# Kernel tuning notes

Measured on AMD Instinct MI355X. Metric: run time of the kernel, lower is better.

Reference implementation:

```python
import jax, jax.numpy as jnp
import numpy as np

N_NODES = 100000
N_EDGES = 1600000
IN_FEATS = 256
OUT_FEATS = 128


def setup_inputs() -> dict:
    key = jax.random.key(0)
    k1, k2, k3, k4 = jax.random.split(key, 4)
    feat = jax.random.normal(k1, (N_NODES, IN_FEATS), dtype=jnp.float32)
    # Glorot-uniform-like weight
    limit = np.sqrt(6.0 / (IN_FEATS + OUT_FEATS)).astype(np.float32)
    weight = jax.random.uniform(k2, (IN_FEATS, OUT_FEATS), dtype=jnp.float32,
                                minval=-limit, maxval=limit)
    bias = jnp.zeros((OUT_FEATS,), dtype=jnp.float32)
    src = jax.random.randint(k3, (N_EDGES,), 0, N_NODES, dtype=jnp.int32)
    dst = jax.random.randint(k4, (N_EDGES,), 0, N_NODES, dtype=jnp.int32)
    return {"feat": feat, "weight": weight, "bias": bias, "src": src, "dst": dst}


def reference(feat, weight, bias, src, dst):
    n = feat.shape[0]
    # in-degree per node (edges point src -> dst), clipped to >= 1
    deg = jax.ops.segment_sum(jnp.ones_like(dst, dtype=feat.dtype), dst,
                              num_segments=n)
    norm = jnp.clip(deg, 1.0, None) ** -0.5          # [N]
    norm = norm[:, None]                             # [N, 1]
    h = feat * norm                                  # src-side normalization
    # in_feats > out_feats: project first, then aggregate (cheaper messages)
    h = h @ weight                                   # [N, out]
    agg = jax.ops.segment_sum(h[src], dst, num_segments=n)  # sparse sum-aggregate
    rst = agg * norm + bias                          # dst-side norm + bias
    return rst
```

## Files before the change

### kernel.cpp

```cpp
#include <hip/hip_runtime.h>

#define IN_F 256
#define OUT_F 128
#define BSH 7
#define BNODES 128
#define MAXBUCK 1024
#define BIN1A_BLOCKS 256
#define BIN1B_BLOCKS 256

typedef short bf16x8 __attribute__((ext_vector_type(8)));
typedef float f32x4 __attribute__((ext_vector_type(4)));

__device__ inline unsigned short f2bf(float x) {
    union { float f; unsigned u; } v; v.f = x;
    unsigned r = v.u + 0x7FFFu + ((v.u >> 16) & 1u);
    return (unsigned short)(r >> 16);
}
__device__ inline float bf2f(unsigned short x) {
    union { unsigned u; float f; } v; v.u = ((unsigned)x) << 16;
    return v.f;
}

__global__ __launch_bounds__(256) void prep_kernel(const float* __restrict__ W,
                                                   unsigned short* __restrict__ Wt,
                                                   const int* __restrict__ dst,
                                                   int* __restrict__ bhist,
                                                   int n_edges, int nbuck) {
    if ((int)blockIdx.x < BIN1A_BLOCKS) {
        __shared__ int hist[MAXBUCK];
        const int tid = threadIdx.x;
        const int chunk = (n_edges + BIN1A_BLOCKS - 1) / BIN1A_BLOCKS;
        const int lo = blockIdx.x * chunk;
        const int hi = min(lo + chunk, n_edges);

        for (int i = tid; i < MAXBUCK; i += 256) hist[i] = 0;
        __syncthreads();
        for (int e = lo + tid; e < hi; e += 256)
            atomicAdd(&hist[dst[e] >> BSH], 1);
        __syncthreads();
        for (int i = tid; i < nbuck; i += 256) {
            int c = hist[i];
            if (c) atomicAdd(&bhist[i], c);
        }
    } else {
        int n = blockIdx.x - BIN1A_BLOCKS;
        int k = threadIdx.x;
        Wt[n * IN_F + k] = f2bf(W[k * OUT_F + n]);
    }
}

__global__ __launch_bounds__(1024) void scanb_kernel(const int* __restrict__ bhist,
                                                     int* __restrict__ bstart,
                                                     int* __restrict__ gcur,
                                                     int* __restrict__ rstart,
                                                     int nbuck, int n_nodes) {
    __shared__ int sh[1024];
    int tid = threadIdx.x;
    int v = (tid < nbuck) ? bhist[tid] : 0;
    sh[tid] = v;
    __syncthreads();
    #pragma unroll
    for (int off = 1; off < 1024; off <<= 1) {
        int t = (tid >= off) ? sh[tid - off] : 0;
        __syncthreads();
        sh[tid] += t;
        __syncthreads();
    }
    int ex = sh[tid] - v;
    if (tid < nbuck) { bstart[tid] = ex; gcur[tid] = ex; }
    if (tid == 1023) {
        bstart[nbuck] = sh[1023];
        rstart[n_nodes] = sh[1023];
    }
}

__global__ __launch_bounds__(512) void gemm_bin_kernel(
        const float* __restrict__ feat, const unsigned short* __restrict__ Wt,
        unsigned short* __restrict__ h, int n_nodes,
        const int* __restrict__ src, const int* __restrict__ dst,
        int* __restrict__ gcur, unsigned* __restrict__ ebuf,
        int n_edges, int nbuck) {

    __shared__ __align__(16) char smem[65536];

    if ((int)blockIdx.x < BIN1B_BLOCKS) {
        int* hist  = (int*)smem;
        int* lbase = hist + MAXBUCK;
        const int tid = threadIdx.x;
        const int chunk = (n_edges + BIN1B_BLOCKS - 1) / BIN1B_BLOCKS;
        const int lo = blockIdx.x * chunk;
        const int hi = min(lo + chunk, n_edges);

        for (int i = tid; i < nbuck; i += 512) hist[i] = 0;
        __syncthreads();
        for (int e = lo + tid; e < hi; e += 512)
            atomicAdd(&hist[dst[e] >> BSH], 1);
        __syncthreads();
        for (int i = tid; i < nbuck; i += 512) {
            int c = hist[i];
            lbase[i] = (c > 0) ? atomicAdd(&gcur[i], c) : 0;
            hist[i] = 0;
        }
        __syncthreads();
        for (int e = lo + tid; e < hi; e += 512) {
            int d = dst[e];
            int bkt = d >> BSH;
            int off = atomicAdd(&hist[bkt], 1);
            ebuf[lbase[bkt] + off] = ((unsigned)src[e] << BSH) | (unsigned)(d & (BNODES - 1));
        }
    } else {
        unsigned short* Bs = (unsigned short*)smem;

        const int tid  = threadIdx.x;
        const int wave = tid >> 6;
        const int lane = tid & 63;
        const int gb   = blockIdx.x - BIN1B_BLOCKS;
        const int r0   = (gb * 8 + wave) * 16;
        const int lrow = lane & 15;
        const int g    = lane >> 4;
        const int kgrp = g * 8;

        {
            const f32x4* srcv = reinterpret_cast<const f32x4*>(Wt);
            f32x4* dstv = reinterpret_cast<f32x4*>(Bs);
            #pragma unroll
            for (int i = 0; i < 8; ++i) {
                int c   = tid + i * 512;
                int row = c >> 5;
                int col = c & 31;
                dstv[c] = srcv[row * 32 + (col ^ (row & 7))];
            }
        }

        const int row  = r0 + lrow;
        const int rowc = (row < n_nodes) ? row : (n_nodes - 1);
        const float* arow = feat + (size_t)rowc * IN_F;

        f32x4 a[16];
        #pragma unroll
        for (int k0 = 0; k0 < IN_F / 32; ++k0) {
            a[2 * k0]     = *reinterpret_cast<const f32x4*>(arow + k0 * 32 + kgrp);
            a[2 * k0 + 1] = *reinterpret_cast<const f32x4*>(arow + k0 * 32 + kgrp + 4);
        }
        asm volatile("" ::
            "v"(a[0]),  "v"(a[1]),  "v"(a[2]),  "v"(a[3]),
            "v"(a[4]),  "v"(a[5]),  "v"(a[6]),  "v"(a[7]),
            "v"(a[8]),  "v"(a[9]),  "v"(a[10]), "v"(a[11]),
            "v"(a[12]), "v"(a[13]), "v"(a[14]), "v"(a[15]));

        __syncthreads();

        f32x4 acc[8];
        #pragma unroll
        for (int n = 0; n < 8; ++n) acc[n] = (f32x4){0.f, 0.f, 0.f, 0.f};

        const bf16x8* bsv = reinterpret_cast<const bf16x8*>(Bs);

        #pragma unroll
        for (int k0 = 0; k0 < IN_F / 32; ++k0) {
            const f32x4 a0 = a[2 * k0];
            const f32x4 a1 = a[2 * k0 + 1];
            bf16x8 afr;
            afr[0] = (short)f2bf(a0[0]);
            afr[1] = (short)f2bf(a0[1]);
            afr[2] = (short)f2bf(a0[2]);
            afr[3] = (short)f2bf(a0[3]);
            afr[4] = (short)f2bf(a1[0]);
            afr[5] = (short)f2bf(a1[1]);
            afr[6] = (short)f2bf(a1[2]);
            afr[7] = (short)f2bf(a1[3]);
            #pragma unroll
            for (int n = 0; n < 8; ++n) {
                const int brow = n * 16 + lrow;
                bf16x8 bfr = bsv[brow * 32 + ((k0 * 4 + g) ^ (brow & 7))];
                acc[n] = __builtin_amdgcn_mfma_f32_16x16x32_bf16(afr, bfr, acc[n], 0, 0, 0);
            }
        }

        const int orow0 = r0 + g * 4;
        #pragma unroll
        for (int n = 0; n < 8; ++n) {
            #pragma unroll
            for (int j = 0; j < 4; ++j) {
                int orow = orow0 + j;
                if (orow < n_nodes)
                    h[(size_t)orow * OUT_F + n * 16 + lrow] = f2bf(acc[n][j]);
            }
        }
    }
}

__global__ __launch_bounds__(256) void bin2_kernel(const unsigned* __restrict__ ebuf,
                                                   const int* __restrict__ bstart,
                                                   int* __restrict__ rstart,
                                                   float* __restrict__ norm,
                                                   int* __restrict__ eidx,
                                                   int n_nodes) {
    __shared__ int lcnt[BNODES];
    __shared__ int lex[BNODES];
    const int tid = threadIdx.x;
    const int node0 = blockIdx.x << BSH;
    const int e0 = bstart[blockIdx.x];
    const int e1 = bstart[blockIdx.x + 1];

    if (tid < BNODES) lcnt[tid] = 0;
    __syncthreads();
    for (int e = e0 + tid; e < e1; e += 256)
        atomicAdd(&lcnt[ebuf[e] & (BNODES - 1)], 1);
    __syncthreads();

    int own = (tid < BNODES) ? lcnt[tid] : 0;
    if (tid < BNODES) lex[tid] = own;
    __syncthreads();
    #pragma unroll
    for (int off = 1; off < BNODES; off <<= 1) {
        int t = (tid >= off && tid < BNODES) ? lex[tid - off] : 0;
        __syncthreads();
        if (tid < BNODES) lex[tid] += t;
        __syncthreads();
    }
    if (tid < BNODES) {
        int ex = lex[tid] - own;
        lex[tid] = ex;
        int g = node0 + tid;
        if (g <= n_nodes) rstart[g] = e0 + ex;
        if (g < n_nodes) {
            float d = (float)own;
            if (d < 1.0f) d = 1.0f;
            norm[g] = 1.0f / sqrtf(d);
        }
        lcnt[tid] = 0;
    }
    __syncthreads();

    for (int e = e0 + tid; e < e1; e += 256) {
        unsigned pk = ebuf[e];
        int dl = pk & (BNODES - 1);
        int pos = atomicAdd(&lcnt[dl], 1);
        eidx[e0 + lex[dl] + pos] = (int)(pk >> BSH);
    }
}

__global__ __launch_bounds__(256) void agg_kernel(const unsigned short* __restrict__ h,
                                                  const int* __restrict__ eidx,
                                                  const int* __restrict__ rstart,
                                                  const float* __restrict__ norm,
                                                  const float* __restrict__ bias,
                                                  float* __restrict__ out,
                                                  int n_nodes) {
    const int wave = threadIdx.x >> 6;
    const int lane = threadIdx.x & 63;
    const int node = blockIdx.x * 4 + wave;
    if (node >= n_nodes) return;

    const int start = rstart[node];
    const int cnt   = rstart[node + 1] - start;

    float a0 = 0.f, a1 = 0.f;
    for (int base = 0; base < cnt; base += 64) {
        const int rem = min(64, cnt - base);
        int   ev = (lane < rem) ? eidx[start + base + lane] : 0;
        float nv = (lane < rem) ? norm[ev] : 0.f;

        int j = 0;
        for (; j + 8 <= rem; j += 8) {
            unsigned v[8];
            float    nn[8];
            #pragma unroll
            for (int q = 0; q < 8; ++q) {
                int s = __shfl(ev, j + q);
                nn[q] = __shfl(nv, j + q);
                v[q]  = *reinterpret_cast<const unsigned*>(h + (size_t)s * OUT_F + lane * 2);
            }
            #pragma unroll
            for (int q = 0; q < 8; ++q) {
                a0 += bf2f((unsigned short)(v[q] & 0xffffu)) * nn[q];
                a1 += bf2f((unsigned short)(v[q] >> 16))     * nn[q];
            }
        }
        for (; j < rem; ++j) {
            int   s  = __shfl(ev, j);
            float nm = __shfl(nv, j);
            unsigned v = *reinterpret_cast<const unsigned*>(h + (size_t)s * OUT_F + lane * 2);
            a0 += bf2f((unsigned short)(v & 0xffffu)) * nm;
            a1 += bf2f((unsigned short)(v >> 16))     * nm;
        }
    }

    const float nd = norm[node];
    float2 r;
    r.x = a0 * nd + bias[lane * 2];
    r.y = a1 * nd + bias[lane * 2 + 1];
    *reinterpret_cast<float2*>(out + (size_t)node * OUT_F + lane * 2) = r;
}

extern "C" void kernel_launch(void* const* d_in, const int* in_sizes, int n_in,
                              void* d_out, int out_size, void* d_ws, size_t ws_size,
                              hipStream_t stream) {
    const float* feat   = (const float*)d_in[0];
    const float* weight = (const float*)d_in[1];
    const float* bias   = (const float*)d_in[2];
    const int*   src    = (const int*)d_in[3];
    const int*   dst    = (const int*)d_in[4];
    float* out = (float*)d_out;

    const int n_nodes = in_sizes[0] / IN_F;
    const int n_edges = in_sizes[3];
    const int nbuck   = (n_nodes + BNODES - 1) >> BSH;
    const int gemm_blocks = (n_nodes + 127) / 128;

    char* ws = (char*)d_ws;
    size_t off = 0;
    auto alloc = [&](size_t bytes) {
        char* p = ws + off;
        off += (bytes + 15) & ~(size_t)15;
        return p;
    };
    unsigned short* h  = (unsigned short*)alloc((size_t)n_nodes * OUT_F * 2);
    float* norm        = (float*)alloc((size_t)n_nodes * 4);
    int*   rstart      = (int*)alloc(((size_t)n_nodes + 1) * 4);
    int*   bhist       = (int*)alloc(MAXBUCK * 4);
    int*   bstart      = (int*)alloc((MAXBUCK + 1) * 4);
    int*   gcur        = (int*)alloc(MAXBUCK * 4);
    unsigned short* Wt = (unsigned short*)alloc((size_t)OUT_F * IN_F * 2);
    unsigned* ebuf     = (unsigned*)alloc((size_t)n_edges * 4);
    int*   eidx        = (int*)alloc((size_t)n_edges * 4);

    hipMemsetAsync(bhist, 0, MAXBUCK * sizeof(int), stream);
    prep_kernel<<<BIN1A_BLOCKS + OUT_F, 256, 0, stream>>>(weight, Wt, dst, bhist,
                                                          n_edges, nbuck);
    scanb_kernel<<<1, 1024, 0, stream>>>(bhist, bstart, gcur, rstart, nbuck, n_nodes);
    gemm_bin_kernel<<<BIN1B_BLOCKS + gemm_blocks, 512, 0, stream>>>(
        feat, Wt, h, n_nodes, src, dst, gcur, ebuf, n_edges, nbuck);
    bin2_kernel<<<nbuck, 256, 0, stream>>>(ebuf, bstart, rstart, norm, eidx, n_nodes);
    agg_kernel<<<(n_nodes + 3) / 4, 256, 0, stream>>>(h, eidx, rstart, norm, bias, out, n_nodes);
}
```

Before: 157.0 us.

## Split fused bin/GEMM kernel into separate binning and 1024-thread GEMM kernels

Separates the edge-binning pass and the MFMA projection into two sequential kernels instead of one fused launch that ran them concurrently on disjoint block ranges. The GEMM now uses 1024-thread blocks covering 256 rows, so each staged copy of the weight tile in shared memory serves more rows. It also loads feature rows inside the k-loop instead of prefetching them all into registers. This gives up the overlap between binning and GEMM and may expose more load latency, in exchange for simpler kernels with lower register pressure and less weight staging.

```diff
diff --git a/kernel.cpp b/kernel.cpp
--- a/kernel.cpp
+++ b/kernel.cpp
@@ -74,118 +74,104 @@
     }
 }
 
-__global__ __launch_bounds__(512) void gemm_bin_kernel(
-        const float* __restrict__ feat, const unsigned short* __restrict__ Wt,
-        unsigned short* __restrict__ h, int n_nodes,
-        const int* __restrict__ src, const int* __restrict__ dst,
-        int* __restrict__ gcur, unsigned* __restrict__ ebuf,
-        int n_edges, int nbuck) {
-
-    __shared__ __align__(16) char smem[65536];
-
-    if ((int)blockIdx.x < BIN1B_BLOCKS) {
-        int* hist  = (int*)smem;
-        int* lbase = hist + MAXBUCK;
-        const int tid = threadIdx.x;
-        const int chunk = (n_edges + BIN1B_BLOCKS - 1) / BIN1B_BLOCKS;
-        const int lo = blockIdx.x * chunk;
-        const int hi = min(lo + chunk, n_edges);
-
-        for (int i = tid; i < nbuck; i += 512) hist[i] = 0;
-        __syncthreads();
-        for (int e = lo + tid; e < hi; e += 512)
-            atomicAdd(&hist[dst[e] >> BSH], 1);
-        __syncthreads();
-        for (int i = tid; i < nbuck; i += 512) {
-            int c = hist[i];
-            lbase[i] = (c > 0) ? atomicAdd(&gcur[i], c) : 0;
-            hist[i] = 0;
-        }
-        __syncthreads();
-        for (int e = lo + tid; e < hi; e += 512) {
-            int d = dst[e];
-            int bkt = d >> BSH;
-            int off = atomicAdd(&hist[bkt], 1);
-            ebuf[lbase[bkt] + off] = ((unsigned)src[e] << BSH) | (unsigned)(d & (BNODES - 1));
-        }
-    } else {
-        unsigned short* Bs = (unsigned short*)smem;
-
-        const int tid  = threadIdx.x;
-        const int wave = tid >> 6;
-        const int lane = tid & 63;
-        const int gb   = blockIdx.x - BIN1B_BLOCKS;
-        const int r0   = (gb * 8 + wave) * 16;
-        const int lrow = lane & 15;
-        const int g    = lane >> 4;
-        const int kgrp = g * 8;
-
-        {
-            const f32x4* srcv = reinterpret_cast<const f32x4*>(Wt);
-            f32x4* dstv = reinterpret_cast<f32x4*>(Bs);
-            #pragma unroll
-            for (int i = 0; i < 8; ++i) {
-                int c   = tid + i * 512;
-                int row = c >> 5;
-                int col = c & 31;
-                dstv[c] = srcv[row * 32 + (col ^ (row & 7))];
-            }
-        }
-
-        const int row  = r0 + lrow;
-        const int rowc = (row < n_nodes) ? row : (n_nodes - 1);
-        const float* arow = feat + (size_t)rowc * IN_F;
-
-        f32x4 a[16];
+__global__ __launch_bounds__(256) void bin1b_kernel(const int* __restrict__ src,
+                                                    const int* __restrict__ dst,
+                                                    int* __restrict__ gcur,
+                                                    unsigned* __restrict__ ebuf,
+                                                    int n_edges, int nbuck) {
+    __shared__ int hist[MAXBUCK];
+    __shared__ int lbase[MAXBUCK];
+    const int tid = threadIdx.x;
+    const int chunk = (n_edges + BIN1B_BLOCKS - 1) / BIN1B_BLOCKS;
+    const int lo = blockIdx.x * chunk;
+    const int hi = min(lo + chunk, n_edges);
+
+    for (int i = tid; i < nbuck; i += 256) hist[i] = 0;
+    __syncthreads();
+    for (int e = lo + tid; e < hi; e += 256)
+        atomicAdd(&hist[dst[e] >> BSH], 1);
+    __syncthreads();
+    for (int i = tid; i < nbuck; i += 256) {
+        int c = hist[i];
+        lbase[i] = (c > 0) ? atomicAdd(&gcur[i], c) : 0;
+        hist[i] = 0;
+    }
+    __syncthreads();
+    for (int e = lo + tid; e < hi; e += 256) {
+        int d = dst[e];
+        int bkt = d >> BSH;
+        int off = atomicAdd(&hist[bkt], 1);
+        ebuf[lbase[bkt] + off] = ((unsigned)src[e] << BSH) | (unsigned)(d & (BNODES - 1));
+    }
+}
+
+__global__ __launch_bounds__(1024) void gemm_mfma(const float* __restrict__ feat,
+                                                  const unsigned short* __restrict__ Wt,
+                                                  unsigned short* __restrict__ h,
+                                                  int n_nodes) {
+    __shared__ unsigned short Bs[OUT_F * IN_F];
+
+    const int tid  = threadIdx.x;
+    const int wave = tid >> 6;
+    const int lane = tid & 63;
+    const int r0   = (blockIdx.x * 16 + wave) * 16;
+    const int lrow = lane & 15;
+    const int g    = lane >> 4;
+    const int kgrp = g * 8;
+
+    {
+        const f32x4* srcv = reinterpret_cast<const f32x4*>(Wt);
+        f32x4* dstv = reinterpret_cast<f32x4*>(Bs);
         #pragma unroll
-        for (int k0 = 0; k0 < IN_F / 32; ++k0) {
-            a[2 * k0]     = *reinterpret_cast<const f32x4*>(arow + k0 * 32 + kgrp);
-            a[2 * k0 + 1] = *reinterpret_cast<const f32x4*>(arow + k0 * 32 + kgrp + 4);
-        }
-        asm volatile("" ::
-            "v"(a[0]),  "v"(a[1]),  "v"(a[2]),  "v"(a[3]),
-            "v"(a[4]),  "v"(a[5]),  "v"(a[6]),  "v"(a[7]),
-            "v"(a[8]),  "v"(a[9]),  "v"(a[10]), "v"(a[11]),
-            "v"(a[12]), "v"(a[13]), "v"(a[14]), "v"(a[15]));
-
-        __syncthreads();
-
-        f32x4 acc[8];
-        #pragma unroll
-        for (int n = 0; n < 8; ++n) acc[n] = (f32x4){0.f, 0.f, 0.f, 0.f};
-
-        const bf16x8* bsv = reinterpret_cast<const bf16x8*>(Bs);
-
-        #pragma unroll
-        for (int k0 = 0; k0 < IN_F / 32; ++k0) {
-            const f32x4 a0 = a[2 * k0];
-            const f32x4 a1 = a[2 * k0 + 1];
-            bf16x8 afr;
-            afr[0] = (short)f2bf(a0[0]);
-            afr[1] = (short)f2bf(a0[1]);
-            afr[2] = (short)f2bf(a0[2]);
-            afr[3] = (short)f2bf(a0[3]);
-            afr[4] = (short)f2bf(a1[0]);
-            afr[5] = (short)f2bf(a1[1]);
-            afr[6] = (short)f2bf(a1[2]);
-            afr[7] = (short)f2bf(a1[3]);
-            #pragma unroll
-            for (int n = 0; n < 8; ++n) {
-                const int brow = n * 16 + lrow;
-                bf16x8 bfr = bsv[brow * 32 + ((k0 * 4 + g) ^ (brow & 7))];
-                acc[n] = __builtin_amdgcn_mfma_f32_16x16x32_bf16(afr, bfr, acc[n], 0, 0, 0);
-            }
-        }
-
-        const int orow0 = r0 + g * 4;
+        for (int i = 0; i < 4; ++i) {
+            int c   = tid + i * 1024;
+            int row = c >> 5;
+            int col = c & 31;
+            dstv[c] = srcv[row * 32 + (col ^ (row & 7))];
+        }
+    }
+
+    const int row  = r0 + lrow;
+    const int rowc = (row < n_nodes) ? row : (n_nodes - 1);
+    const float* arow = feat + (size_t)rowc * IN_F;
+
+    __syncthreads();
+
+    f32x4 acc[8];
+    #pragma unroll
+    for (int n = 0; n < 8; ++n) acc[n] = (f32x4){0.f, 0.f, 0.f, 0.f};
+
+    const bf16x8* bsv = reinterpret_cast<const bf16x8*>(Bs);
+
+    #pragma unroll
+    for (int k0 = 0; k0 < IN_F / 32; ++k0) {
+        const f32x4 a0 = *reinterpret_cast<const f32x4*>(arow + k0 * 32 + kgrp);
+        const f32x4 a1 = *reinterpret_cast<const f32x4*>(arow + k0 * 32 + kgrp + 4);
+        bf16x8 afr;
+        afr[0] = (short)f2bf(a0[0]);
+        afr[1] = (short)f2bf(a0[1]);
+        afr[2] = (short)f2bf(a0[2]);
+        afr[3] = (short)f2bf(a0[3]);
+        afr[4] = (short)f2bf(a1[0]);
+        afr[5] = (short)f2bf(a1[1]);
+        afr[6] = (short)f2bf(a1[2]);
+        afr[7] = (short)f2bf(a1[3]);
         #pragma unroll
         for (int n = 0; n < 8; ++n) {
-            #pragma unroll
-            for (int j = 0; j < 4; ++j) {
-                int orow = orow0 + j;
-                if (orow < n_nodes)
-                    h[(size_t)orow * OUT_F + n * 16 + lrow] = f2bf(acc[n][j]);
-            }
+            const int brow = n * 16 + lrow;
+            bf16x8 bfr = bsv[brow * 32 + ((k0 * 4 + g) ^ (brow & 7))];
+            acc[n] = __builtin_amdgcn_mfma_f32_16x16x32_bf16(afr, bfr, acc[n], 0, 0, 0);
+        }
+    }
+
+    const int orow0 = r0 + g * 4;
+    #pragma unroll
+    for (int n = 0; n < 8; ++n) {
+        #pragma unroll
+        for (int j = 0; j < 4; ++j) {
+            int orow = orow0 + j;
+            if (orow < n_nodes)
+                h[(size_t)orow * OUT_F + n * 16 + lrow] = f2bf(acc[n][j]);
         }
     }
 }
@@ -307,7 +293,7 @@
     const int n_nodes = in_sizes[0] / IN_F;
     const int n_edges = in_sizes[3];
     const int nbuck   = (n_nodes + BNODES - 1) >> BSH;
-    const int gemm_blocks = (n_nodes + 127) / 128;
+    const int gemm_blocks = (n_nodes + 255) / 256;
 
     char* ws = (char*)d_ws;
     size_t off = 0;
@@ -330,8 +316,8 @@
     prep_kernel<<<BIN1A_BLOCKS + OUT_F, 256, 0, stream>>>(weight, Wt, dst, bhist,
                                                           n_edges, nbuck);
     scanb_kernel<<<1, 1024, 0, stream>>>(bhist, bstart, gcur, rstart, nbuck, n_nodes);
-    gemm_bin_kernel<<<BIN1B_BLOCKS + gemm_blocks, 512, 0, stream>>>(
-        feat, Wt, h, n_nodes, src, dst, gcur, ebuf, n_edges, nbuck);
+    bin1b_kernel<<<BIN1B_BLOCKS, 256, 0, stream>>>(src, dst, gcur, ebuf, n_edges, nbuck);
+    gemm_mfma<<<gemm_blocks, 1024, 0, stream>>>(feat, Wt, h, n_nodes);
     bin2_kernel<<<nbuck, 256, 0, stream>>>(ebuf, bstart, rstart, norm, eidx, n_nodes);
     agg_kernel<<<(n_nodes + 3) / 4, 256, 0, stream>>>(h, eidx, rstart, norm, bias, out, n_nodes);
 }
```

Result: no change. 159.9 us (+1.8%).
